# Kernel tuning notes

Measured on AMD Instinct MI355X. Metric: run time of the kernel, lower is better.

## Reference

```python
import jax, jax.numpy as jnp
import numpy as np

NUM_FEATURE = 50


def setup_inputs() -> dict:
    key = jax.random.key(0)
    k1, = jax.random.split(key, 1)
    T = 500000
    query = jax.random.normal(k1, (T, NUM_FEATURE), dtype=jnp.float32)
    # Learned params exactly as the torch module initializes them:
    # ql.weight filled with 1 (shape [1, 50] -> we keep [50]), qW scalar 1.0
    ql_w = jnp.ones((NUM_FEATURE,), dtype=jnp.float32)
    qW = jnp.asarray(1.0, dtype=jnp.float32)
    return {"query": query, "ql_w": ql_w, "qW": qW}


def reference(query, ql_w, qW):
    # scores[i] = ql(tanh(qW * query[i]))  -> [T]
    scores = jnp.tanh(qW * query) @ ql_w
    # alpha = softmax(scores) over the T dimension (stable, single pass)
    alpha = jax.nn.softmax(scores, axis=0)
    # z = sum_i alpha[i] * query[i]  -> [NUM_FEATURE]
    z = alpha @ query
    return z
```

## Files before the change

kernel.cpp:

```cpp
#include <hip/hip_runtime.h>
#include <math.h>

#define NF 50
#define REC 52
#define NBLK 1024
#define GRP_PER_BLK 32

__device__ __forceinline__ float fast_tanh(float x) {
    float e = __expf(2.0f * x);
    float r = __builtin_amdgcn_rcpf(e + 1.0f);
    return 1.0f - 2.0f * r;
}

__global__ __launch_bounds__(512, 8) void attn_pass1(
    const float* __restrict__ query, const float* __restrict__ ql_w,
    const float* __restrict__ qWp, float* __restrict__ ws,
    int T, int totalGroups)
{
    const float qW = qWp[0];
    const int tid  = threadIdx.x;
    const int j    = tid & 15;
    const int gIn  = tid >> 4;
    const int gGlob = blockIdx.x * GRP_PER_BLK + gIn;

    float wA0 = 0.f, wA1 = 0.f, wB0 = 0.f, wB1 = 0.f;
    if (j < 13) { wA0 = ql_w[2*j];     wA1 = ql_w[2*j+1]; }
    if (j < 12) { wB0 = ql_w[26+2*j];  wB1 = ql_w[27+2*j]; }

    float m = -1e30f, s = 0.0f;
    float z0 = 0.f, z1 = 0.f, z2 = 0.f, z3 = 0.f;

    const int stride = totalGroups;
    int row = gGlob;
    for (; row + stride < T; row += 2 * stride) {
        const float2* q0 = (const float2*)(query + (size_t)row * NF);
        const float2* q1 = (const float2*)(query + (size_t)(row + stride) * NF);
        float2 a0 = make_float2(0.f,0.f), b0 = make_float2(0.f,0.f);
        float2 a1 = make_float2(0.f,0.f), b1 = make_float2(0.f,0.f);
        if (j < 13) { a0 = q0[j];     a1 = q1[j]; }
        if (j < 12) { b0 = q0[13+j];  b1 = q1[13+j]; }

        float p0 = fmaf(fast_tanh(qW*a0.x), wA0, fmaf(fast_tanh(qW*a0.y), wA1,
                   fmaf(fast_tanh(qW*b0.x), wB0, fast_tanh(qW*b0.y)*wB1)));
        float p1 = fmaf(fast_tanh(qW*a1.x), wA0, fmaf(fast_tanh(qW*a1.y), wA1,
                   fmaf(fast_tanh(qW*b1.x), wB0, fast_tanh(qW*b1.y)*wB1)));
        p0 += __shfl_xor(p0, 1);  p1 += __shfl_xor(p1, 1);
        p0 += __shfl_xor(p0, 2);  p1 += __shfl_xor(p1, 2);
        p0 += __shfl_xor(p0, 4);  p1 += __shfl_xor(p1, 4);
        p0 += __shfl_xor(p0, 8);  p1 += __shfl_xor(p1, 8);
        const float sc0 = p0, sc1 = p1;

        float mn = fmaxf(fmaxf(m, sc0), sc1);
        float c  = __expf(m - mn);
        float e0 = __expf(sc0 - mn);
        float e1 = __expf(sc1 - mn);
        s  = fmaf(s, c, e0 + e1);
        z0 = fmaf(e0, a0.x, fmaf(e1, a1.x, z0 * c));
        z1 = fmaf(e0, a0.y, fmaf(e1, a1.y, z1 * c));
        z2 = fmaf(e0, b0.x, fmaf(e1, b1.x, z2 * c));
        z3 = fmaf(e0, b0.y, fmaf(e1, b1.y, z3 * c));
        m = mn;
    }
    if (row < T) {
        const float2* q0 = (const float2*)(query + (size_t)row * NF);
        float2 a0 = make_float2(0.f,0.f), b0 = make_float2(0.f,0.f);
        if (j < 13) a0 = q0[j];
        if (j < 12) b0 = q0[13+j];
        float p0 = fmaf(fast_tanh(qW*a0.x), wA0, fmaf(fast_tanh(qW*a0.y), wA1,
                   fmaf(fast_tanh(qW*b0.x), wB0, fast_tanh(qW*b0.y)*wB1)));
        p0 += __shfl_xor(p0, 1);
        p0 += __shfl_xor(p0, 2);
        p0 += __shfl_xor(p0, 4);
        p0 += __shfl_xor(p0, 8);
        float mn = fmaxf(m, p0);
        float c  = __expf(m - mn);
        float e0 = __expf(p0 - mn);
        s  = fmaf(s, c, e0);
        z0 = fmaf(e0, a0.x, z0 * c);
        z1 = fmaf(e0, a0.y, z1 * c);
        z2 = fmaf(e0, b0.x, z2 * c);
        z3 = fmaf(e0, b0.y, z3 * c);
        m = mn;
    }

    __shared__ float sm[GRP_PER_BLK], ss[GRP_PER_BLK];
    __shared__ float sz[GRP_PER_BLK][REC];
    if (j == 0) { sm[gIn] = m; ss[gIn] = s; }
    if (j < 13) { sz[gIn][2*j]    = z0; sz[gIn][2*j+1]  = z1; }
    if (j < 12) { sz[gIn][26+2*j] = z2; sz[gIn][27+2*j] = z3; }
    __syncthreads();

    if (tid < NF) {
        float M = sm[0];
        #pragma unroll
        for (int h = 1; h < GRP_PER_BLK; ++h) M = fmaxf(M, sm[h]);
        float S = 0.f, Z = 0.f;
        #pragma unroll
        for (int h = 0; h < GRP_PER_BLK; ++h) {
            float e = __expf(sm[h] - M);
            S += ss[h] * e;
            Z += sz[h][tid] * e;
        }
        float* rec = ws + (size_t)blockIdx.x * REC;
        rec[tid] = Z;
        if (tid == 0) { rec[50] = M; rec[51] = S; }
    }
}

__global__ __launch_bounds__(1024) void attn_pass2(
    const float* __restrict__ ws, float* __restrict__ out, int B)
{
    __shared__ float e_lds[NBLK];
    __shared__ float red[1024];
    __shared__ float zacc[16][REC];
    const int tid = threadIdx.x;

    float mv = -1e30f, sv = 0.f;
    if (tid < B) {
        float2 ms = *(const float2*)(ws + (size_t)tid * REC + 50);
        mv = ms.x; sv = ms.y;
    }
    red[tid] = mv;
    __syncthreads();
    #pragma unroll
    for (int st = 512; st > 0; st >>= 1) {
        if (tid < st) red[tid] = fmaxf(red[tid], red[tid + st]);
        __syncthreads();
    }
    const float M = red[0];
    __syncthreads();

    float e = __expf(mv - M);
    e_lds[tid] = e;
    red[tid] = sv * e;
    __syncthreads();
    #pragma unroll
    for (int st = 512; st > 0; st >>= 1) {
        if (tid < st) red[tid] += red[tid + st];
        __syncthreads();
    }
    const float S = red[0];

    const int w = tid >> 6, lane = tid & 63;
    float acc = 0.f;
    if (lane < REC) {
        int b = w;
        for (; b + 112 < B; b += 128) {
            float v0 = ws[(size_t)(b      ) * REC + lane];
            float v1 = ws[(size_t)(b +  16) * REC + lane];
            float v2 = ws[(size_t)(b +  32) * REC + lane];
            float v3 = ws[(size_t)(b +  48) * REC + lane];
            float v4 = ws[(size_t)(b +  64) * REC + lane];
            float v5 = ws[(size_t)(b +  80) * REC + lane];
            float v6 = ws[(size_t)(b +  96) * REC + lane];
            float v7 = ws[(size_t)(b + 112) * REC + lane];
            acc += v0 * e_lds[b]      + v1 * e_lds[b +  16]
                 + v2 * e_lds[b + 32] + v3 * e_lds[b +  48]
                 + v4 * e_lds[b + 64] + v5 * e_lds[b +  80]
                 + v6 * e_lds[b + 96] + v7 * e_lds[b + 112];
        }
        for (; b < B; b += 16)
            acc += ws[(size_t)b * REC + lane] * e_lds[b];
        zacc[w][lane] = acc;
    }
    __syncthreads();
    if (tid < NF) {
        float Z = 0.f;
        #pragma unroll
        for (int h = 0; h < 16; ++h) Z += zacc[h][tid];
        out[tid] = Z / S;
    }
}

extern "C" void kernel_launch(void* const* d_in, const int* in_sizes, int n_in,
                              void* d_out, int out_size, void* d_ws, size_t ws_size,
                              hipStream_t stream) {
    const float* query = (const float*)d_in[0];
    const float* ql_w  = (const float*)d_in[1];
    const float* qW    = (const float*)d_in[2];
    float* out = (float*)d_out;
    float* ws  = (float*)d_ws;

    const int T = in_sizes[0] / NF;

    int B = NBLK;
    size_t need = (size_t)B * REC * sizeof(float);
    if (ws_size < need) {
        B = (int)(ws_size / (REC * sizeof(float)));
        if (B < 1) B = 1;
    }

    const int totalGroups = B * GRP_PER_BLK;
    hipLaunchKernelGGL(attn_pass1, dim3(B), dim3(512), 0, stream,
                       query, ql_w, qW, ws, T, totalGroups);
    hipLaunchKernelGGL(attn_pass2, dim3(1), dim3(1024), 0, stream,
                       ws, out, B);
}
```

Measured before the change: 31.26 us.

## Replace online softmax with static bound shift and DPP row reductions

Since tanh is bounded, the score is bounded by the sum of |w|. The kernel therefore drops the running max and rescaling and computes exp(score - bound) directly, rewriting tanh so that score = sumW - 2*sum(w*rcp(exp(2x)+1)). The pass2 max reduction goes away; partial sums are simply added. Row reductions switch from shuffles to DPP row_shr ops, and the main loop is unrolled to 4 rows. The fixed shift could underflow when weights are large, which the 80 clamp only partly guards against.

```diff
diff --git a/kernel.cpp b/kernel.cpp
--- a/kernel.cpp
+++ b/kernel.cpp
@@ -5,11 +5,24 @@
 #define REC 52
 #define NBLK 1024
 #define GRP_PER_BLK 32
+#define LOG2E 1.44269504f
 
-__device__ __forceinline__ float fast_tanh(float x) {
-    float e = __expf(2.0f * x);
-    float r = __builtin_amdgcn_rcpf(e + 1.0f);
-    return 1.0f - 2.0f * r;
+__device__ __forceinline__ float row16_allsum(float v) {
+    float t;
+    t = __int_as_float(__builtin_amdgcn_update_dpp(0, __float_as_int(v), 0x121, 0xF, 0xF, true)); v += t;
+    t = __int_as_float(__builtin_amdgcn_update_dpp(0, __float_as_int(v), 0x122, 0xF, 0xF, true)); v += t;
+    t = __int_as_float(__builtin_amdgcn_update_dpp(0, __float_as_int(v), 0x124, 0xF, 0xF, true)); v += t;
+    t = __int_as_float(__builtin_amdgcn_update_dpp(0, __float_as_int(v), 0x128, 0xF, 0xF, true)); v += t;
+    return v;
+}
+
+__device__ __forceinline__ float row_partial(float2 a, float2 b, float c2,
+                                             float wA0, float wA1, float wB0, float wB1) {
+    float r0 = __builtin_amdgcn_rcpf(__builtin_amdgcn_exp2f(c2 * a.x) + 1.f);
+    float r1 = __builtin_amdgcn_rcpf(__builtin_amdgcn_exp2f(c2 * a.y) + 1.f);
+    float r2 = __builtin_amdgcn_rcpf(__builtin_amdgcn_exp2f(c2 * b.x) + 1.f);
+    float r3 = __builtin_amdgcn_rcpf(__builtin_amdgcn_exp2f(c2 * b.y) + 1.f);
+    return fmaf(wA0, r0, fmaf(wA1, r1, fmaf(wB0, r2, wB1 * r3)));
 }
 
 __global__ __launch_bounds__(512, 8) void attn_pass1(
@@ -27,147 +40,106 @@
     if (j < 13) { wA0 = ql_w[2*j];     wA1 = ql_w[2*j+1]; }
     if (j < 12) { wB0 = ql_w[26+2*j];  wB1 = ql_w[27+2*j]; }
 
-    float m = -1e30f, s = 0.0f;
-    float z0 = 0.f, z1 = 0.f, z2 = 0.f, z3 = 0.f;
+    const float sumAbsW = row16_allsum(fabsf(wA0)+fabsf(wA1)+fabsf(wB0)+fabsf(wB1));
+    const float sumW    = row16_allsum(wA0 + wA1 + wB0 + wB1);
+    const float M0 = (sumAbsW > 80.f) ? (sumAbsW - 80.f) : 0.f;
+    const float c2 = 2.f * qW * LOG2E;
+    const float K  = (sumW - M0) * LOG2E;
+    const float n2l = -2.f * LOG2E;
+
+    float s = 0.f, z0 = 0.f, z1 = 0.f, z2 = 0.f, z3 = 0.f;
 
     const int stride = totalGroups;
     int row = gGlob;
-    for (; row + stride < T; row += 2 * stride) {
+    for (; row + 3*stride < T; row += 4*stride) {
         const float2* q0 = (const float2*)(query + (size_t)row * NF);
-        const float2* q1 = (const float2*)(query + (size_t)(row + stride) * NF);
+        const float2* q1 = (const float2*)(query + (size_t)(row +   stride) * NF);
+        const float2* q2 = (const float2*)(query + (size_t)(row + 2*stride) * NF);
+        const float2* q3 = (const float2*)(query + (size_t)(row + 3*stride) * NF);
         float2 a0 = make_float2(0.f,0.f), b0 = make_float2(0.f,0.f);
         float2 a1 = make_float2(0.f,0.f), b1 = make_float2(0.f,0.f);
-        if (j < 13) { a0 = q0[j];     a1 = q1[j]; }
-        if (j < 12) { b0 = q0[13+j];  b1 = q1[13+j]; }
+        float2 a2 = make_float2(0.f,0.f), b2 = make_float2(0.f,0.f);
+        float2 a3 = make_float2(0.f,0.f), b3 = make_float2(0.f,0.f);
+        if (j < 13) { a0 = q0[j];    a1 = q1[j];    a2 = q2[j];    a3 = q3[j]; }
+        if (j < 12) { b0 = q0[13+j]; b1 = q1[13+j]; b2 = q2[13+j]; b3 = q3[13+j]; }
 
-        float p0 = fmaf(fast_tanh(qW*a0.x), wA0, fmaf(fast_tanh(qW*a0.y), wA1,
-                   fmaf(fast_tanh(qW*b0.x), wB0, fast_tanh(qW*b0.y)*wB1)));
-        float p1 = fmaf(fast_tanh(qW*a1.x), wA0, fmaf(fast_tanh(qW*a1.y), wA1,
-                   fmaf(fast_tanh(qW*b1.x), wB0, fast_tanh(qW*b1.y)*wB1)));
-        p0 += __shfl_xor(p0, 1);  p1 += __shfl_xor(p1, 1);
-        p0 += __shfl_xor(p0, 2);  p1 += __shfl_xor(p1, 2);
-        p0 += __shfl_xor(p0, 4);  p1 += __shfl_xor(p1, 4);
-        p0 += __shfl_xor(p0, 8);  p1 += __shfl_xor(p1, 8);
-        const float sc0 = p0, sc1 = p1;
+        float p0 = row_partial(a0, b0, c2, wA0, wA1, wB0, wB1);
+        float p1 = row_partial(a1, b1, c2, wA0, wA1, wB0, wB1);
+        float p2 = row_partial(a2, b2, c2, wA0, wA1, wB0, wB1);
+        float p3 = row_partial(a3, b3, c2, wA0, wA1, wB0, wB1);
+        p0 = row16_allsum(p0);
+        p1 = row16_allsum(p1);
+        p2 = row16_allsum(p2);
+        p3 = row16_allsum(p3);
+        float e0 = __builtin_amdgcn_exp2f(fmaf(p0, n2l, K));
+        float e1 = __builtin_amdgcn_exp2f(fmaf(p1, n2l, K));
+        float e2 = __builtin_amdgcn_exp2f(fmaf(p2, n2l, K));
+        float e3 = __builtin_amdgcn_exp2f(fmaf(p3, n2l, K));
 
-        float mn = fmaxf(fmaxf(m, sc0), sc1);
-        float c  = __expf(m - mn);
-        float e0 = __expf(sc0 - mn);
-        float e1 = __expf(sc1 - mn);
-        s  = fmaf(s, c, e0 + e1);
-        z0 = fmaf(e0, a0.x, fmaf(e1, a1.x, z0 * c));
-        z1 = fmaf(e0, a0.y, fmaf(e1, a1.y, z1 * c));
-        z2 = fmaf(e0, b0.x, fmaf(e1, b1.x, z2 * c));
-        z3 = fmaf(e0, b0.y, fmaf(e1, b1.y, z3 * c));
-        m = mn;
+        s += (e0 + e1) + (e2 + e3);
+        z0 = fmaf(e0, a0.x, fmaf(e1, a1.x, fmaf(e2, a2.x, fmaf(e3, a3.x, z0))));
+        z1 = fmaf(e0, a0.y, fmaf(e1, a1.y, fmaf(e2, a2.y, fmaf(e3, a3.y, z1))));
+        z2 = fmaf(e0, b0.x, fmaf(e1, b1.x, fmaf(e2, b2.x, fmaf(e3, b3.x, z2))));
+        z3 = fmaf(e0, b0.y, fmaf(e1, b1.y, fmaf(e2, b2.y, fmaf(e3, b3.y, z3))));
     }
-    if (row < T) {
+    for (; row < T; row += stride) {
         const float2* q0 = (const float2*)(query + (size_t)row * NF);
-        float2 a0 = make_float2(0.f,0.f), b0 = make_float2(0.f,0.f);
-        if (j < 13) a0 = q0[j];
-        if (j < 12) b0 = q0[13+j];
-        float p0 = fmaf(fast_tanh(qW*a0.x), wA0, fmaf(fast_tanh(qW*a0.y), wA1,
-                   fmaf(fast_tanh(qW*b0.x), wB0, fast_tanh(qW*b0.y)*wB1)));
-        p0 += __shfl_xor(p0, 1);
-        p0 += __shfl_xor(p0, 2);
-        p0 += __shfl_xor(p0, 4);
-        p0 += __shfl_xor(p0, 8);
-        float mn = fmaxf(m, p0);
-        float c  = __expf(m - mn);
-        float e0 = __expf(p0 - mn);
-        s  = fmaf(s, c, e0);
-        z0 = fmaf(e0, a0.x, z0 * c);
-        z1 = fmaf(e0, a0.y, z1 * c);
-        z2 = fmaf(e0, b0.x, z2 * c);
-        z3 = fmaf(e0, b0.y, z3 * c);
-        m = mn;
+        float2 a = make_float2(0.f,0.f), b = make_float2(0.f,0.f);
+        if (j < 13) a = q0[j];
+        if (j < 12) b = q0[13+j];
+        float p = row_partial(a, b, c2, wA0, wA1, wB0, wB1);
+        p = row16_allsum(p);
+        float e = __builtin_amdgcn_exp2f(fmaf(p, n2l, K));
+        s += e;
+        z0 = fmaf(e, a.x, z0);
+        z1 = fmaf(e, a.y, z1);
+        z2 = fmaf(e, b.x, z2);
+        z3 = fmaf(e, b.y, z3);
     }
 
-    __shared__ float sm[GRP_PER_BLK], ss[GRP_PER_BLK];
     __shared__ float sz[GRP_PER_BLK][REC];
-    if (j == 0) { sm[gIn] = m; ss[gIn] = s; }
     if (j < 13) { sz[gIn][2*j]    = z0; sz[gIn][2*j+1]  = z1; }
     if (j < 12) { sz[gIn][26+2*j] = z2; sz[gIn][27+2*j] = z3; }
+    if (j == 13) { sz[gIn][50] = s; sz[gIn][51] = 0.f; }
     __syncthreads();
 
-    if (tid < NF) {
-        float M = sm[0];
+    if (tid < 51) {
+        float acc = 0.f;
         #pragma unroll
-        for (int h = 1; h < GRP_PER_BLK; ++h) M = fmaxf(M, sm[h]);
-        float S = 0.f, Z = 0.f;
-        #pragma unroll
-        for (int h = 0; h < GRP_PER_BLK; ++h) {
-            float e = __expf(sm[h] - M);
-            S += ss[h] * e;
-            Z += sz[h][tid] * e;
-        }
-        float* rec = ws + (size_t)blockIdx.x * REC;
-        rec[tid] = Z;
-        if (tid == 0) { rec[50] = M; rec[51] = S; }
+        for (int h = 0; h < GRP_PER_BLK; ++h) acc += sz[h][tid];
+        ws[(size_t)blockIdx.x * REC + tid] = acc;
     }
 }
 
 __global__ __launch_bounds__(1024) void attn_pass2(
     const float* __restrict__ ws, float* __restrict__ out, int B)
 {
-    __shared__ float e_lds[NBLK];
-    __shared__ float red[1024];
     __shared__ float zacc[16][REC];
     const int tid = threadIdx.x;
+    const int w = tid >> 6, lane = tid & 63;
 
-    float mv = -1e30f, sv = 0.f;
-    if (tid < B) {
-        float2 ms = *(const float2*)(ws + (size_t)tid * REC + 50);
-        mv = ms.x; sv = ms.y;
-    }
-    red[tid] = mv;
-    __syncthreads();
-    #pragma unroll
-    for (int st = 512; st > 0; st >>= 1) {
-        if (tid < st) red[tid] = fmaxf(red[tid], red[tid + st]);
-        __syncthreads();
-    }
-    const float M = red[0];
-    __syncthreads();
-
-    float e = __expf(mv - M);
-    e_lds[tid] = e;
-    red[tid] = sv * e;
-    __syncthreads();
-    #pragma unroll
-    for (int st = 512; st > 0; st >>= 1) {
-        if (tid < st) red[tid] += red[tid + st];
-        __syncthreads();
-    }
-    const float S = red[0];
-
-    const int w = tid >> 6, lane = tid & 63;
-    float acc = 0.f;
-    if (lane < REC) {
+    if (lane < 51) {
+        float acc = 0.f;
         int b = w;
         for (; b + 112 < B; b += 128) {
-            float v0 = ws[(size_t)(b      ) * REC + lane];
-            float v1 = ws[(size_t)(b +  16) * REC + lane];
-            float v2 = ws[(size_t)(b +  32) * REC + lane];
-            float v3 = ws[(size_t)(b +  48) * REC + lane];
-            float v4 = ws[(size_t)(b +  64) * REC + lane];
-            float v5 = ws[(size_t)(b +  80) * REC + lane];
-            float v6 = ws[(size_t)(b +  96) * REC + lane];
-            float v7 = ws[(size_t)(b + 112) * REC + lane];
-            acc += v0 * e_lds[b]      + v1 * e_lds[b +  16]
-                 + v2 * e_lds[b + 32] + v3 * e_lds[b +  48]
-                 + v4 * e_lds[b + 64] + v5 * e_lds[b +  80]
-                 + v6 * e_lds[b + 96] + v7 * e_lds[b + 112];
+            acc += ws[(size_t)(b      ) * REC + lane]
+                 + ws[(size_t)(b +  16) * REC + lane]
+                 + ws[(size_t)(b +  32) * REC + lane]
+                 + ws[(size_t)(b +  48) * REC + lane]
+                 + ws[(size_t)(b +  64) * REC + lane]
+                 + ws[(size_t)(b +  80) * REC + lane]
+                 + ws[(size_t)(b +  96) * REC + lane]
+                 + ws[(size_t)(b + 112) * REC + lane];
         }
         for (; b < B; b += 16)
-            acc += ws[(size_t)b * REC + lane] * e_lds[b];
+            acc += ws[(size_t)b * REC + lane];
         zacc[w][lane] = acc;
     }
     __syncthreads();
     if (tid < NF) {
-        float Z = 0.f;
+        float Z = 0.f, S = 0.f;
         #pragma unroll
-        for (int h = 0; h < 16; ++h) Z += zacc[h][tid];
+        for (int h = 0; h < 16; ++h) { Z += zacc[h][tid]; S += zacc[h][50]; }
         out[tid] = Z / S;
     }
 }
```

Result: faster. 28.37 us (-9.3%).
